# Optimization experiments

Hardware: AMD Instinct MI355X
Metric: run time of the kernel (lower is better)

Reference implementation:

```python
import jax, jax.numpy as jnp
import numpy as np

EMBED_DIM = 1024
NUM_HEADS = 16
HEAD_DIM = EMBED_DIM // NUM_HEADS
SCALING = HEAD_DIM ** -0.5
TGT, BSZ = 1024, 4


def setup_inputs() -> dict:
    key = jax.random.key(0)
    ks = jax.random.split(key, 8)
    query = jax.random.normal(ks[0], (TGT, BSZ, EMBED_DIM), dtype=jnp.float32)
    key_padding_mask = jax.random.randint(ks[1], (BSZ, TGT), 0, 2, dtype=jnp.int32)
    attn_mask = jax.random.normal(ks[2], (TGT, TGT), dtype=jnp.float32)
    attn_bias = jax.random.normal(ks[3], (BSZ * NUM_HEADS, TGT, TGT), dtype=jnp.float32)
    W_in = jax.random.normal(ks[4], (3 * EMBED_DIM, EMBED_DIM), dtype=jnp.float32) * 0.02
    b_in = jnp.zeros((3 * EMBED_DIM,), dtype=jnp.float32)
    W_out = jax.random.normal(ks[5], (EMBED_DIM, EMBED_DIM), dtype=jnp.float32) * 0.02
    b_out = jnp.zeros((EMBED_DIM,), dtype=jnp.float32)
    return {"query": query, "key_padding_mask": key_padding_mask,
            "attn_mask": attn_mask, "attn_bias": attn_bias,
            "W_in": W_in, "b_in": b_in, "W_out": W_out, "b_out": b_out}


def reference(query, key_padding_mask, attn_mask, attn_bias, W_in, b_in, W_out, b_out):
    tgt_len, bsz, embed_dim = query.shape
    # in_proj: (T,B,C) @ W_in.T -> (T,B,3C), chunk into q,k,v
    qkv = jnp.einsum('tbc,ec->tbe', query, W_in) + b_in
    q, k, v = jnp.split(qkv, 3, axis=-1)
    # reshape to (B*H, T, D)
    def to_bh(x):
        return x.reshape(tgt_len, bsz * NUM_HEADS, HEAD_DIM).transpose(1, 0, 2)
    q = to_bh(q) * SCALING
    k = to_bh(k)
    v = to_bh(v)
    src_len = k.shape[1]
    # scores: (B*H, T, S)
    attn_weights = jnp.einsum('ntd,nsd->nts', q, k)
    attn_weights = attn_weights + attn_mask[None, :, :]
    kpm = key_padding_mask.astype(bool)  # (B, S), True = pad
    aw = attn_weights.reshape(bsz, NUM_HEADS, tgt_len, src_len)
    aw = jnp.where(kpm[:, None, None, :], -jnp.inf, aw)
    attn_weights = aw.reshape(bsz * NUM_HEADS, tgt_len, src_len)
    attn_weights = attn_weights + attn_bias
    attn_probs = jax.nn.softmax(attn_weights, axis=-1)
    attn = jnp.einsum('nts,nsd->ntd', attn_probs, v)
    attn = attn.transpose(1, 0, 2).reshape(tgt_len, bsz, embed_dim)
    out = jnp.einsum('tbc,ec->tbe', attn, W_out) + b_out
    return out
```

## Files before the change

kernel.cpp:

```cpp
#include <hip/hip_runtime.h>

#define T_LEN 1024
#define B_SZ 4
#define EMB 1024
#define NH 16
#define HD 64
#define QKV_LD 3072

typedef _Float16 f16;
typedef __attribute__((ext_vector_type(8))) _Float16 f16x8;
typedef __attribute__((ext_vector_type(4))) _Float16 f16x4;
typedef __attribute__((ext_vector_type(4))) float f32x4;

__device__ __forceinline__ void gload16(const f16* g, f16* l) {
    __builtin_amdgcn_global_load_lds(
        (const __attribute__((address_space(1))) void*)g,
        (__attribute__((address_space(3))) void*)l, 16, 0, 0);
}

__global__ __launch_bounds__(256) void cvt_f32_to_f16(
    const float* __restrict__ in, f16* __restrict__ out, int n4)
{
    int i = blockIdx.x * 256 + threadIdx.x;
    if (i < n4) {
        float4 v = ((const float4*)in)[i];
        f16x4 h = { (f16)v.x, (f16)v.y, (f16)v.z, (f16)v.w };
        ((f16x4*)out)[i] = h;
    }
}

template<bool OUT_HALF>
__global__ __launch_bounds__(256) void gemm_ct(
    const f16* __restrict__ Wt, const f16* __restrict__ Xa,
    const float* __restrict__ bias, void* __restrict__ Out,
    int K, int ldo)
{
    __shared__ f16 As[128 * 32];
    __shared__ f16 Bs[128 * 32];
    const int tid = threadIdx.x;
    const int wv = tid >> 6, lane = tid & 63;
    const int lq = lane & 15, quad = lane >> 4;
    const int m0 = blockIdx.x * 128, n0 = blockIdx.y * 128;
    const int wm = (wv >> 1) * 64, wn = (wv & 1) * 64;

    const int s1 = tid, s2 = 256 + tid;
    const f16* a1 = Wt + (size_t)(m0 + (s1 >> 2)) * K + (s1 & 3) * 8;
    const f16* a2 = Wt + (size_t)(m0 + (s2 >> 2)) * K + (s2 & 3) * 8;
    const f16* b1 = Xa + (size_t)(n0 + (s1 >> 2)) * K + (s1 & 3) * 8;
    const f16* b2 = Xa + (size_t)(n0 + (s2 >> 2)) * K + (s2 & 3) * 8;
    f16* lA1 = As + s1 * 8; f16* lA2 = As + s2 * 8;
    f16* lB1 = Bs + s1 * 8; f16* lB2 = Bs + s2 * 8;

    f32x4 acc[4][4];
#pragma unroll
    for (int i = 0; i < 4; ++i)
#pragma unroll
        for (int j = 0; j < 4; ++j) acc[i][j] = (f32x4){0.f, 0.f, 0.f, 0.f};

    for (int k0 = 0; k0 < K; k0 += 32) {
        __syncthreads();
        gload16(a1 + k0, lA1);
        gload16(a2 + k0, lA2);
        gload16(b1 + k0, lB1);
        gload16(b2 + k0, lB2);
        __syncthreads();
        f16x8 af[4], bf[4];
#pragma unroll
        for (int t = 0; t < 4; ++t) {
            af[t] = *(const f16x8*)&As[(wm + t * 16 + lq) * 32 + quad * 8];
            bf[t] = *(const f16x8*)&Bs[(wn + t * 16 + lq) * 32 + quad * 8];
        }
#pragma unroll
        for (int mt = 0; mt < 4; ++mt)
#pragma unroll
            for (int nt = 0; nt < 4; ++nt)
                acc[mt][nt] = __builtin_amdgcn_mfma_f32_16x16x32_f16(
                    af[mt], bf[nt], acc[mt][nt], 0, 0, 0);
    }

#pragma unroll
    for (int mt = 0; mt < 4; ++mt) {
        const int e0 = m0 + wm + mt * 16 + quad * 4;
        const float4 bb = *(const float4*)(bias + e0);
#pragma unroll
        for (int nt = 0; nt < 4; ++nt) {
            const int xr = n0 + wn + nt * 16 + lq;
            if (OUT_HALF) {
                f16x4 h = { (f16)(acc[mt][nt][0] + bb.x), (f16)(acc[mt][nt][1] + bb.y),
                            (f16)(acc[mt][nt][2] + bb.z), (f16)(acc[mt][nt][3] + bb.w) };
                *(f16x4*)((f16*)Out + (size_t)xr * ldo + e0) = h;
            } else {
                float4 o = { acc[mt][nt][0] + bb.x, acc[mt][nt][1] + bb.y,
                             acc[mt][nt][2] + bb.z, acc[mt][nt][3] + bb.w };
                *(float4*)((float*)Out + (size_t)xr * ldo + e0) = o;
            }
        }
    }
}

__global__ __launch_bounds__(256) void vtrans(
    const f16* __restrict__ qkv, f16* __restrict__ Vth)
{
    __shared__ f16 Ls[256 * 66];
    const int bh = blockIdx.x;
    const int t0 = blockIdx.y * 256;
    const int b = bh >> 4, hh = bh & 15;
    const int tid = threadIdx.x;

#pragma unroll
    for (int p = 0; p < 8; ++p) {
        const int g = p * 2048 + tid * 8;
        const int ti = g >> 6, dj = g & 63;
        f16x8 v = *(const f16x8*)(qkv + (size_t)((t0 + ti) * 4 + b) * QKV_LD + 2048 + hh * 64 + dj);
        *(f16x8*)&Ls[ti * 66 + dj] = v;
    }
    __syncthreads();
#pragma unroll
    for (int p = 0; p < 8; ++p) {
        const int g = p * 2048 + tid * 8;
        const int d = g >> 8, tt = g & 255;
        f16x8 o;
#pragma unroll
        for (int j = 0; j < 8; ++j) o[j] = Ls[(tt + j) * 66 + d];
        *(f16x8*)(Vth + (size_t)bh * 65536 + (size_t)d * 1024 + t0 + tt) = o;
    }
}

__global__ __launch_bounds__(256) void attn_v3(
    const f16* __restrict__ qkv, const f16* __restrict__ Vth,
    const int* __restrict__ kpm, const float* __restrict__ attn_mask,
    const float* __restrict__ attn_bias, f16* __restrict__ ctx)
{
    const int LDP = 72;
    __shared__ f16 Ps[4 * 16 * LDP];

    const int tid = threadIdx.x;
    const int wv = tid >> 6, lane = tid & 63;
    const int lq = lane & 15, quad = lane >> 4;
    const int q0 = blockIdx.x * 64;
    const int bh = blockIdx.y;
    const int b = bh >> 4, hh = bh & 15;
    f16* Pw = Ps + wv * 16 * LDP;

    const int t = q0 + wv * 16 + lq;
    const float* mrow = attn_mask + (size_t)t * T_LEN;
    const float* brow = attn_bias + ((size_t)bh * T_LEN + t) * T_LEN;
    const int* kpr = kpm + b * T_LEN;
    const f16* Vb = Vth + (size_t)bh * 65536;

    f16x8 bq[2];
    {
        const f16* qrow = qkv + (size_t)(t * 4 + b) * QKV_LD + hh * 64;
        bq[0] = *(const f16x8*)(qrow + quad * 8);
        bq[1] = *(const f16x8*)(qrow + 32 + quad * 8);
    }

    float m_i = -1e30f, l_i = 0.0f;
    f32x4 O[4];
#pragma unroll
    for (int dt = 0; dt < 4; ++dt) O[dt] = (f32x4){0.f, 0.f, 0.f, 0.f};

    float4 b4[4];
#pragma unroll
    for (int st = 0; st < 4; ++st)
        b4[st] = *(const float4*)(brow + st * 16 + quad * 4);

    for (int s0 = 0; s0 < T_LEN; s0 += 64) {
        f16x8 ak[2][4];
#pragma unroll
        for (int ks = 0; ks < 2; ++ks)
#pragma unroll
            for (int st = 0; st < 4; ++st)
                ak[ks][st] = *(const f16x8*)(qkv
                    + (size_t)((s0 + st * 16 + lq) * 4 + b) * QKV_LD
                    + EMB + hh * 64 + ks * 32 + quad * 8);
        f16x8 av[2][4];
#pragma unroll
        for (int ks = 0; ks < 2; ++ks)
#pragma unroll
            for (int dt = 0; dt < 4; ++dt)
                av[ks][dt] = *(const f16x8*)(Vb + (size_t)(dt * 16 + lq) * 1024
                                             + s0 + ks * 32 + quad * 8);
        float4 m4[4]; int4 kp4[4];
#pragma unroll
        for (int st = 0; st < 4; ++st) {
            const int sb = s0 + st * 16 + quad * 4;
            m4[st] = *(const float4*)(mrow + sb);
            kp4[st] = *(const int4*)(kpr + sb);
        }
        float4 b4n[4];
        if (s0 + 64 < T_LEN) {
#pragma unroll
            for (int st = 0; st < 4; ++st)
                b4n[st] = *(const float4*)(brow + s0 + 64 + st * 16 + quad * 4);
        }

        f32x4 sacc[4];
#pragma unroll
        for (int st = 0; st < 4; ++st) sacc[st] = (f32x4){0.f, 0.f, 0.f, 0.f};
#pragma unroll
        for (int ks = 0; ks < 2; ++ks)
#pragma unroll
            for (int st = 0; st < 4; ++st)
                sacc[st] = __builtin_amdgcn_mfma_f32_16x16x32_f16(
                    ak[ks][st], bq[ks], sacc[st], 0, 0, 0);

        float sv[4][4];
        float rm = -1e30f;
#pragma unroll
        for (int st = 0; st < 4; ++st) {
            const float mv[4] = {m4[st].x, m4[st].y, m4[st].z, m4[st].w};
            const float bv[4] = {b4[st].x, b4[st].y, b4[st].z, b4[st].w};
            const int kv[4] = {kp4[st].x, kp4[st].y, kp4[st].z, kp4[st].w};
#pragma unroll
            for (int r = 0; r < 4; ++r) {
                const float x = sacc[st][r] * 0.125f + mv[r] + bv[r];
                sv[st][r] = kv[r] ? -1e30f : x;
                rm = fmaxf(rm, sv[st][r]);
            }
        }
        rm = fmaxf(rm, __shfl_xor(rm, 16));
        rm = fmaxf(rm, __shfl_xor(rm, 32));
        const float mn = fmaxf(m_i, rm);
        const float alpha = __expf(m_i - mn);
        m_i = mn;

        __builtin_amdgcn_wave_barrier();
        float rs = 0.0f;
#pragma unroll
        for (int st = 0; st < 4; ++st) {
            f16x4 pv;
#pragma unroll
            for (int r = 0; r < 4; ++r) {
                const float p = __expf(sv[st][r] - mn);
                rs += p;
                pv[r] = (f16)p;
            }
            *(f16x4*)&Pw[lq * LDP + st * 16 + quad * 4] = pv;
        }
        rs += __shfl_xor(rs, 16);
        rs += __shfl_xor(rs, 32);
        l_i = l_i * alpha + rs;

        float aB[4];
#pragma unroll
        for (int r = 0; r < 4; ++r) aB[r] = __shfl(alpha, quad * 4 + r, 16);
#pragma unroll
        for (int dt = 0; dt < 4; ++dt)
#pragma unroll
            for (int r = 0; r < 4; ++r) O[dt][r] *= aB[r];

        __builtin_amdgcn_wave_barrier();

#pragma unroll
        for (int ks = 0; ks < 2; ++ks) {
            const f16x8 ap = *(const f16x8*)&Pw[lq * LDP + ks * 32 + quad * 8];
#pragma unroll
            for (int dt = 0; dt < 4; ++dt)
                O[dt] = __builtin_amdgcn_mfma_f32_16x16x32_f16(
                    ap, av[ks][dt], O[dt], 0, 0, 0);
        }

#pragma unroll
        for (int st = 0; st < 4; ++st) b4[st] = b4n[st];
    }

    float lB[4];
#pragma unroll
    for (int r = 0; r < 4; ++r) lB[r] = __shfl(l_i, quad * 4 + r, 16);
#pragma unroll
    for (int r = 0; r < 4; ++r) {
        const float inv = 1.0f / lB[r];
        const int tt = q0 + wv * 16 + quad * 4 + r;
#pragma unroll
        for (int dt = 0; dt < 4; ++dt)
            ctx[((size_t)tt * B_SZ + b) * EMB + hh * HD + dt * 16 + lq] = (f16)(O[dt][r] * inv);
    }
}

extern "C" void kernel_launch(void* const* d_in, const int* in_sizes, int n_in,
                              void* d_out, int out_size, void* d_ws, size_t ws_size,
                              hipStream_t stream)
{
    const float* query     = (const float*)d_in[0];
    const int*   kpm       = (const int*)  d_in[1];
    const float* attn_mask = (const float*)d_in[2];
    const float* attn_bias = (const float*)d_in[3];
    const float* W_in      = (const float*)d_in[4];
    const float* b_in      = (const float*)d_in[5];
    const float* W_out     = (const float*)d_in[6];
    const float* b_out     = (const float*)d_in[7];
    float* out = (float*)d_out;

    f16* q16    = (f16*)d_ws;
    f16* win16  = q16    + (size_t)4096 * 1024;
    f16* wout16 = win16  + (size_t)3072 * 1024;
    f16* qkv16  = wout16 + (size_t)1024 * 1024;
    f16* Vth    = qkv16  + (size_t)4096 * 3072;
    f16* ctx16  = Vth    + (size_t)64 * 65536;

    cvt_f32_to_f16<<<4096 * 1024 / 1024, 256, 0, stream>>>(query, q16,    4096 * 1024 / 4);
    cvt_f32_to_f16<<<3072 * 1024 / 1024, 256, 0, stream>>>(W_in,  win16,  3072 * 1024 / 4);
    cvt_f32_to_f16<<<1024 * 1024 / 1024, 256, 0, stream>>>(W_out, wout16, 1024 * 1024 / 4);

    dim3 g1(3072 / 128, 4096 / 128);
    gemm_ct<true><<<g1, 256, 0, stream>>>(win16, q16, b_in, qkv16, 1024, QKV_LD);

    dim3 gv(64, 4);
    vtrans<<<gv, 256, 0, stream>>>(qkv16, Vth);

    dim3 g2(T_LEN / 64, B_SZ * NH);
    attn_v3<<<g2, 256, 0, stream>>>(qkv16, Vth, kpm, attn_mask, attn_bias, ctx16);

    dim3 g3(1024 / 128, 4096 / 128);
    gemm_ct<false><<<g3, 256, 0, stream>>>(wout16, ctx16, b_out, out, 1024, 1024);
}
```

Baseline: 590.5 us.

## Deepen attn_bias prefetch to 128 keys with nontemporal loads and fuse conversions

Three fp32-to-fp16 conversion launches become one kernel that picks its source buffer by index, removing two launches. The attention kernel now prefetches the attn_bias row 128 keys ahead instead of 64, using nontemporal loads. The loop processes two 64-key halves per iteration. The goal is to hide more latency on the 256MB bias stream and avoid polluting the cache with it, at the cost of more registers, which may reduce occupancy.

```diff
diff --git a/kernel.cpp b/kernel.cpp
--- a/kernel.cpp
+++ b/kernel.cpp
@@ -18,15 +18,22 @@
         (__attribute__((address_space(3))) void*)l, 16, 0, 0);
 }
 
-__global__ __launch_bounds__(256) void cvt_f32_to_f16(
-    const float* __restrict__ in, f16* __restrict__ out, int n4)
+#define N4_Q  (4096 * 1024 / 4)
+#define N4_WI (3072 * 1024 / 4)
+#define N4_WO (1024 * 1024 / 4)
+__global__ __launch_bounds__(256) void cvt_all(
+    const float* __restrict__ q, const float* __restrict__ wi,
+    const float* __restrict__ wo, f16* __restrict__ q16,
+    f16* __restrict__ wi16, f16* __restrict__ wo16)
 {
     int i = blockIdx.x * 256 + threadIdx.x;
-    if (i < n4) {
-        float4 v = ((const float4*)in)[i];
-        f16x4 h = { (f16)v.x, (f16)v.y, (f16)v.z, (f16)v.w };
-        ((f16x4*)out)[i] = h;
-    }
+    const float* src; f16* dst; int off;
+    if (i < N4_Q)             { src = q;  dst = q16;  off = i; }
+    else if (i < N4_Q + N4_WI){ src = wi; dst = wi16; off = i - N4_Q; }
+    else                      { src = wo; dst = wo16; off = i - N4_Q - N4_WI; }
+    float4 v = ((const float4*)src)[off];
+    f16x4 h = { (f16)v.x, (f16)v.y, (f16)v.z, (f16)v.w };
+    ((f16x4*)dst)[off] = h;
 }
 
 template<bool OUT_HALF>
@@ -126,7 +133,7 @@
     }
 }
 
-__global__ __launch_bounds__(256) void attn_v3(
+__global__ __launch_bounds__(256) void attn_v4(
     const f16* __restrict__ qkv, const f16* __restrict__ Vth,
     const int* __restrict__ kpm, const float* __restrict__ attn_mask,
     const float* __restrict__ attn_bias, f16* __restrict__ ctx)
@@ -160,109 +167,113 @@
 #pragma unroll
     for (int dt = 0; dt < 4; ++dt) O[dt] = (f32x4){0.f, 0.f, 0.f, 0.f};
 
-    float4 b4[4];
-#pragma unroll
-    for (int st = 0; st < 4; ++st)
-        b4[st] = *(const float4*)(brow + st * 16 + quad * 4);
-
-    for (int s0 = 0; s0 < T_LEN; s0 += 64) {
-        f16x8 ak[2][4];
-#pragma unroll
-        for (int ks = 0; ks < 2; ++ks)
-#pragma unroll
-            for (int st = 0; st < 4; ++st)
-                ak[ks][st] = *(const f16x8*)(qkv
-                    + (size_t)((s0 + st * 16 + lq) * 4 + b) * QKV_LD
-                    + EMB + hh * 64 + ks * 32 + quad * 8);
-        f16x8 av[2][4];
-#pragma unroll
-        for (int ks = 0; ks < 2; ++ks)
+    f32x4 bb[8];
+#pragma unroll
+    for (int j = 0; j < 8; ++j)
+        bb[j] = __builtin_nontemporal_load((const f32x4*)(brow + j * 16 + quad * 4));
+
+    for (int s0 = 0; s0 < T_LEN; s0 += 128) {
+        f32x4 bbn[8];
+#pragma unroll
+        for (int half = 0; half < 2; ++half) {
+            const int sh = s0 + half * 64;
+
+            f16x8 ak[2][4];
+#pragma unroll
+            for (int ks = 0; ks < 2; ++ks)
+#pragma unroll
+                for (int st = 0; st < 4; ++st)
+                    ak[ks][st] = *(const f16x8*)(qkv
+                        + (size_t)((sh + st * 16 + lq) * 4 + b) * QKV_LD
+                        + EMB + hh * 64 + ks * 32 + quad * 8);
+            f16x8 av[2][4];
+#pragma unroll
+            for (int ks = 0; ks < 2; ++ks)
+#pragma unroll
+                for (int dt = 0; dt < 4; ++dt)
+                    av[ks][dt] = *(const f16x8*)(Vb + (size_t)(dt * 16 + lq) * 1024
+                                                 + sh + ks * 32 + quad * 8);
+            f32x4 m4[4]; int4 kp4[4];
+#pragma unroll
+            for (int st = 0; st < 4; ++st) {
+                const int sb = sh + st * 16 + quad * 4;
+                m4[st] = *(const f32x4*)(mrow + sb);
+                kp4[st] = *(const int4*)(kpr + sb);
+            }
+            if (half == 1 && s0 + 128 < T_LEN) {
+#pragma unroll
+                for (int j = 0; j < 8; ++j)
+                    bbn[j] = __builtin_nontemporal_load(
+                        (const f32x4*)(brow + s0 + 128 + j * 16 + quad * 4));
+            }
+
+            f32x4 sacc[4];
+#pragma unroll
+            for (int st = 0; st < 4; ++st) sacc[st] = (f32x4){0.f, 0.f, 0.f, 0.f};
+#pragma unroll
+            for (int ks = 0; ks < 2; ++ks)
+#pragma unroll
+                for (int st = 0; st < 4; ++st)
+                    sacc[st] = __builtin_amdgcn_mfma_f32_16x16x32_f16(
+                        ak[ks][st], bq[ks], sacc[st], 0, 0, 0);
+
+            float sv[4][4];
+            float rm = -1e30f;
+#pragma unroll
+            for (int st = 0; st < 4; ++st) {
+                const f32x4 bv = bb[half * 4 + st];
+                const int kv[4] = {kp4[st].x, kp4[st].y, kp4[st].z, kp4[st].w};
+#pragma unroll
+                for (int r = 0; r < 4; ++r) {
+                    const float x = sacc[st][r] * 0.125f + m4[st][r] + bv[r];
+                    sv[st][r] = kv[r] ? -1e30f : x;
+                    rm = fmaxf(rm, sv[st][r]);
+                }
+            }
+            rm = fmaxf(rm, __shfl_xor(rm, 16));
+            rm = fmaxf(rm, __shfl_xor(rm, 32));
+            const float mn = fmaxf(m_i, rm);
+            const float alpha = __expf(m_i - mn);
+            m_i = mn;
+
+            __builtin_amdgcn_wave_barrier();
+            float rs = 0.0f;
+#pragma unroll
+            for (int st = 0; st < 4; ++st) {
+                f16x4 pv;
+#pragma unroll
+                for (int r = 0; r < 4; ++r) {
+                    const float p = __expf(sv[st][r] - mn);
+                    rs += p;
+                    pv[r] = (f16)p;
+                }
+                *(f16x4*)&Pw[lq * LDP + st * 16 + quad * 4] = pv;
+            }
+            rs += __shfl_xor(rs, 16);
+            rs += __shfl_xor(rs, 32);
+            l_i = l_i * alpha + rs;
+
+            float aB[4];
+#pragma unroll
+            for (int r = 0; r < 4; ++r) aB[r] = __shfl(alpha, quad * 4 + r, 16);
 #pragma unroll
             for (int dt = 0; dt < 4; ++dt)
-                av[ks][dt] = *(const f16x8*)(Vb + (size_t)(dt * 16 + lq) * 1024
-                                             + s0 + ks * 32 + quad * 8);
-        float4 m4[4]; int4 kp4[4];
-#pragma unroll
-        for (int st = 0; st < 4; ++st) {
-            const int sb = s0 + st * 16 + quad * 4;
-            m4[st] = *(const float4*)(mrow + sb);
-            kp4[st] = *(const int4*)(kpr + sb);
+#pragma unroll
+                for (int r = 0; r < 4; ++r) O[dt][r] *= aB[r];
+
+            __builtin_amdgcn_wave_barrier();
+
+#pragma unroll
+            for (int ks = 0; ks < 2; ++ks) {
+                const f16x8 ap = *(const f16x8*)&Pw[lq * LDP + ks * 32 + quad * 8];
+#pragma unroll
+                for (int dt = 0; dt < 4; ++dt)
+                    O[dt] = __builtin_amdgcn_mfma_f32_16x16x32_f16(
+                        ap, av[ks][dt], O[dt], 0, 0, 0);
+            }
         }
-        float4 b4n[4];
-        if (s0 + 64 < T_LEN) {
-#pragma unroll
-            for (int st = 0; st < 4; ++st)
-                b4n[st] = *(const float4*)(brow + s0 + 64 + st * 16 + quad * 4);
-        }
-
-        f32x4 sacc[4];
-#pragma unroll
-        for (int st = 0; st < 4; ++st) sacc[st] = (f32x4){0.f, 0.f, 0.f, 0.f};
-#pragma unroll
-        for (int ks = 0; ks < 2; ++ks)
-#pragma unroll
-            for (int st = 0; st < 4; ++st)
-                sacc[st] = __builtin_amdgcn_mfma_f32_16x16x32_f16(
-                    ak[ks][st], bq[ks], sacc[st], 0, 0, 0);
-
-        float sv[4][4];
-        float rm = -1e30f;
-#pragma unroll
-        for (int st = 0; st < 4; ++st) {
-            const float mv[4] = {m4[st].x, m4[st].y, m4[st].z, m4[st].w};
-            const float bv[4] = {b4[st].x, b4[st].y, b4[st].z, b4[st].w};
-            const int kv[4] = {kp4[st].x, kp4[st].y, kp4[st].z, kp4[st].w};
-#pragma unroll
-            for (int r = 0; r < 4; ++r) {
-                const float x = sacc[st][r] * 0.125f + mv[r] + bv[r];
-                sv[st][r] = kv[r] ? -1e30f : x;
-                rm = fmaxf(rm, sv[st][r]);
-            }
-        }
-        rm = fmaxf(rm, __shfl_xor(rm, 16));
-        rm = fmaxf(rm, __shfl_xor(rm, 32));
-        const float mn = fmaxf(m_i, rm);
-        const float alpha = __expf(m_i - mn);
-        m_i = mn;
-
-        __builtin_amdgcn_wave_barrier();
-        float rs = 0.0f;
-#pragma unroll
-        for (int st = 0; st < 4; ++st) {
-            f16x4 pv;
-#pragma unroll
-            for (int r = 0; r < 4; ++r) {
-                const float p = __expf(sv[st][r] - mn);
-                rs += p;
-                pv[r] = (f16)p;
-            }
-            *(f16x4*)&Pw[lq * LDP + st * 16 + quad * 4] = pv;
-        }
-        rs += __shfl_xor(rs, 16);
-        rs += __shfl_xor(rs, 32);
-        l_i = l_i * alpha + rs;
-
-        float aB[4];
-#pragma unroll
-        for (int r = 0; r < 4; ++r) aB[r] = __shfl(alpha, quad * 4 + r, 16);
-#pragma unroll
-        for (int dt = 0; dt < 4; ++dt)
-#pragma unroll
-            for (int r = 0; r < 4; ++r) O[dt][r] *= aB[r];
-
-        __builtin_amdgcn_wave_barrier();
-
-#pragma unroll
-        for (int ks = 0; ks < 2; ++ks) {
-            const f16x8 ap = *(const f16x8*)&Pw[lq * LDP + ks * 32 + quad * 8];
-#pragma unroll
-            for (int dt = 0; dt < 4; ++dt)
-                O[dt] = __builtin_amdgcn_mfma_f32_16x16x32_f16(
-                    ap, av[ks][dt], O[dt], 0, 0, 0);
-        }
-
-#pragma unroll
-        for (int st = 0; st < 4; ++st) b4[st] = b4n[st];
+#pragma unroll
+        for (int j = 0; j < 8; ++j) bb[j] = bbn[j];
     }
 
     float lB[4];
@@ -299,9 +310,8 @@
     f16* Vth    = qkv16  + (size_t)4096 * 3072;
     f16* ctx16  = Vth    + (size_t)64 * 65536;
 
-    cvt_f32_to_f16<<<4096 * 1024 / 1024, 256, 0, stream>>>(query, q16,    4096 * 1024 / 4);
-    cvt_f32_to_f16<<<3072 * 1024 / 1024, 256, 0, stream>>>(W_in,  win16,  3072 * 1024 / 4);
-    cvt_f32_to_f16<<<1024 * 1024 / 1024, 256, 0, stream>>>(W_out, wout16, 1024 * 1024 / 4);
+    cvt_all<<<(N4_Q + N4_WI + N4_WO) / 256, 256, 0, stream>>>(
+        query, W_in, W_out, q16, win16, wout16);
 
     dim3 g1(3072 / 128, 4096 / 128);
     gemm_ct<true><<<g1, 256, 0, stream>>>(win16, q16, b_in, qkv16, 1024, QKV_LD);
@@ -310,7 +320,7 @@
     vtrans<<<gv, 256, 0, stream>>>(qkv16, Vth);
 
     dim3 g2(T_LEN / 64, B_SZ * NH);
-    attn_v3<<<g2, 256, 0, stream>>>(qkv16, Vth, kpm, attn_mask, attn_bias, ctx16);
+    attn_v4<<<g2, 256, 0, stream>>>(qkv16, Vth, kpm, attn_mask, attn_bias, ctx16);
 
     dim3 g3(1024 / 128, 4096 / 128);
     gemm_ct<false><<<g3, 256, 0, stream>>>(wout16, ctx16, b_out, out, 1024, 1024);
```

New measurement: 586.6 us. Within noise of the previous version (-0.7%).
